# Optimization experiments

Hardware: AMD Instinct MI355X
Metric: run time of the kernel (lower is better)

## Reference

```python
import jax, jax.numpy as jnp
import numpy as np

L, H, D, M = 2, 8, 64, 64   # layers, heads, query dim, value dim
DM = H * M                  # d_model = 512
FF = 1024                   # feed-forward dim
B, S, F_IN = 8, 4096, 586   # batch, seq_len, input feature dim
EPS_ATTN = 1e-6             # fast_transformers LinearAttention eps
EPS_LN = 1e-5               # torch LayerNorm default eps


def setup_inputs() -> dict:
    key = jax.random.key(0)
    ks = jax.random.split(key, 16)
    p = lambda k, shape: jax.random.normal(k, shape, jnp.float32) * 0.02
    return {
        "embeddings": jax.random.normal(ks[0], (B, S, F_IN), jnp.float32),
        "W0": p(ks[1], (F_IN, DM)), "b0": jnp.zeros((DM,), jnp.float32),
        "Wq": p(ks[2], (L, DM, DM)), "bq": jnp.zeros((L, DM), jnp.float32),
        "Wk": p(ks[3], (L, DM, DM)), "bk": jnp.zeros((L, DM), jnp.float32),
        "Wv": p(ks[4], (L, DM, DM)), "bv": jnp.zeros((L, DM), jnp.float32),
        "Wo": p(ks[5], (L, DM, DM)), "bo": jnp.zeros((L, DM), jnp.float32),
        "ln1_s": jnp.ones((L, DM), jnp.float32), "ln1_b": jnp.zeros((L, DM), jnp.float32),
        "W1": p(ks[6], (L, DM, FF)), "b1": jnp.zeros((L, FF), jnp.float32),
        "W2": p(ks[7], (L, FF, DM)), "b2": jnp.zeros((L, DM), jnp.float32),
        "ln2_s": jnp.ones((L, DM), jnp.float32), "ln2_b": jnp.zeros((L, DM), jnp.float32),
        "lnf_s": jnp.ones((DM,), jnp.float32), "lnf_b": jnp.zeros((DM,), jnp.float32),
        "Wout": p(ks[8], (DM, 1)), "bout": jnp.zeros((1,), jnp.float32),
    }


def _ln(x, s, b):
    mu = x.mean(-1, keepdims=True)
    var = ((x - mu) ** 2).mean(-1, keepdims=True)
    return (x - mu) * jax.lax.rsqrt(var + EPS_LN) * s + b


def _feat(x):
    # elu feature map of fast_transformers linear attention
    return jax.nn.elu(x) + 1.0


def reference(embeddings, W0, b0, Wq, bq, Wk, bk, Wv, bv, Wo, bo,
              ln1_s, ln1_b, W1, b1, W2, b2, ln2_s, ln2_b,
              lnf_s, lnf_b, Wout, bout):
    x = embeddings @ W0 + b0                       # [B,S,DM]
    Bn, Sn = x.shape[0], x.shape[1]
    for l in range(L):
        q = _feat((x @ Wq[l] + bq[l]).reshape(Bn, Sn, H, D))
        k = _feat((x @ Wk[l] + bk[l]).reshape(Bn, Sn, H, D))
        v = (x @ Wv[l] + bv[l]).reshape(Bn, Sn, H, M)
        # non-causal linear attention: O(S) in sequence length
        kv = jnp.einsum("bshd,bshm->bhdm", k, v)                    # [B,H,D,M]
        z = 1.0 / (jnp.einsum("blhd,bhd->blh", q, k.sum(1)) + EPS_ATTN)
        a = jnp.einsum("blhd,bhdm,blh->blhm", q, kv, z).reshape(Bn, Sn, DM)
        x = x + a @ Wo[l] + bo[l]                  # residual (dropout=0 eval)
        x = _ln(x, ln1_s[l], ln1_b[l])
        y = jax.nn.relu(x @ W1[l] + b1[l]) @ W2[l] + b2[l]
        x = _ln(x + y, ln2_s[l], ln2_b[l])
    x = _ln(x, lnf_s, lnf_b)                        # final encoder LayerNorm
    return (x @ Wout + bout)[..., 0]                # squeeze -> [B,S]
```

## Files before the change

### kernel.cpp

```cpp
#include <hip/hip_runtime.h>
#include <hip/hip_bf16.h>
#include <math.h>

typedef unsigned short u16;
typedef short s16x8 __attribute__((ext_vector_type(8)));
typedef float f32x4 __attribute__((ext_vector_type(4)));

#define BS_   32768
#define SEQ_  4096
#define DM_   512
#define FF_   1024
#define FIN_  586
#define FINP_ 640
#define PADE  264

__device__ __forceinline__ u16 f2b(float f) {
    __hip_bfloat16 h = __float2bfloat16(f);
    return *reinterpret_cast<u16*>(&h);
}
__device__ __forceinline__ float b2f(u16 h) {
    union { unsigned u; float f; } a; a.u = ((unsigned)h) << 16;
    return a.f;
}

typedef __attribute__((address_space(1))) const unsigned gu32;
typedef __attribute__((address_space(3))) unsigned lu32;
__device__ __forceinline__ void glds16(const void* g, void* l) {
    __builtin_amdgcn_global_load_lds((gu32*)g, (lu32*)l, 16, 0, 0);
}

__device__ __forceinline__ void tr_tile(const float* __restrict__ W, u16* __restrict__ Wt,
                                        int K, int N, int Kpad, int tidx, int ktiles,
                                        float (*t)[33]) {
    int kb = (tidx % ktiles) << 5, nb = (tidx / ktiles) << 5;
    int tx = threadIdx.x, ty = threadIdx.y;
#pragma unroll
    for (int j = 0; j < 32; j += 8) {
        int k = kb + ty + j;
        t[ty + j][tx] = (k < K) ? W[(size_t)k * N + nb + tx] : 0.f;
    }
    __syncthreads();
#pragma unroll
    for (int j = 0; j < 32; j += 8) {
        Wt[(size_t)(nb + ty + j) * Kpad + kb + tx] = f2b(t[tx][ty + j]);
    }
}

__global__ void k_tr_all(const float* __restrict__ W0, const float* __restrict__ Wq,
                         const float* __restrict__ Wk, const float* __restrict__ Wv,
                         const float* __restrict__ Wo, const float* __restrict__ W1,
                         const float* __restrict__ W2,
                         u16* __restrict__ W0t, u16* __restrict__ Wqkv,
                         u16* __restrict__ Wot, u16* __restrict__ W1t,
                         u16* __restrict__ W2t) {
    __shared__ float t[32][33];
    int b = blockIdx.x;
    if (b < 320) { tr_tile(W0, W0t, FIN_, DM_, FINP_, b, 20, t); return; }
    b -= 320;
    int l = b >> 11;
    int r = b & 2047;
    if (r < 768) {
        int sel = r >> 8, ti = r & 255;
        const float* src = sel == 0 ? Wq : (sel == 1 ? Wk : Wv);
        tr_tile(src + (size_t)l * 262144, Wqkv + (size_t)l * 786432 + (size_t)sel * 262144,
                512, 512, 512, ti, 16, t);
    } else if (r < 1024) {
        tr_tile(Wo + (size_t)l * 262144, Wot + (size_t)l * 262144, 512, 512, 512, r - 768, 16, t);
    } else if (r < 1536) {
        tr_tile(W1 + (size_t)l * 524288, W1t + (size_t)l * 524288, 512, 1024, 512, r - 1024, 16, t);
    } else {
        tr_tile(W2 + (size_t)l * 524288, W2t + (size_t)l * 524288, 1024, 512, 1024, r - 1536, 32, t);
    }
}

__global__ __launch_bounds__(256)
void k_emb(const float* __restrict__ E, u16* __restrict__ Ep) {
    const int total8 = BS_ * (FINP_ / 8);
    for (int i = blockIdx.x * 256 + threadIdx.x; i < total8; i += gridDim.x * 256) {
        int rr = i / (FINP_ / 8), c = (i % (FINP_ / 8)) * 8;
        const float* rp = E + (size_t)rr * FIN_ + c;
        s16x8 o;
#pragma unroll
        for (int e = 0; e < 8; ++e) {
            float v = (c + e < FIN_) ? rp[e] : 0.f;
            o[e] = (short)f2b(v);
        }
        *(s16x8*)(Ep + (size_t)rr * FINP_ + c) = o;
    }
}

template<int EPI>
__global__ __launch_bounds__(512, 2)
void k_gemm(const u16* __restrict__ A, const u16* __restrict__ Bt,
            const float* __restrict__ bias0, const float* __restrict__ bias1,
            const float* __restrict__ bias2,
            const u16* __restrict__ resid,
            u16* __restrict__ out0, u16* __restrict__ out1, u16* __restrict__ out2,
            int M, int N, int K, int NT) {
    __shared__ __align__(16) u16 smem[65536];

    const int nwg = gridDim.x;
    const int cpx = nwg >> 3;
    const int wg = (blockIdx.x & 7) * cpx + (blockIdx.x >> 3);
    const int mt = wg / NT, ntl = wg - mt * NT;
    const int m0 = mt << 8, n0 = ntl << 8;
    const int tid = threadIdx.x;
    const int wid = tid >> 6, l = tid & 63;
    const int wr = wid >> 2, wc = wid & 3;
    const int lr = l & 15, lg = l >> 4;

    const int srow = tid >> 3;
    const int gchunk = (((tid & 7) ^ (srow & 7)) & 7) << 3;
    const u16* Abase = A + (size_t)(m0 + srow) * K + gchunk;
    const u16* Bbase = Bt + (size_t)(n0 + srow) * K + gchunk;

    auto stageA = [&](int d, int tt) {
        u16* dst = smem + d * 16384 + tid * 8;
        const u16* src = Abase + (size_t)tt * 64;
#pragma unroll
        for (int hg = 0; hg < 4; ++hg)
            glds16(src + (size_t)(hg * 64) * K, dst + hg * 4096);
    };
    auto stageB = [&](int d, int tt) {
        u16* dst = smem + 32768 + d * 16384 + tid * 8;
        const u16* src = Bbase + (size_t)tt * 64;
#pragma unroll
        for (int hg = 0; hg < 4; ++hg)
            glds16(src + (size_t)(hg * 64) * K, dst + hg * 4096);
    };

    const int aswz0 = ((0 + lg) ^ (lr & 7)) << 3;
    const int aswz1 = ((4 + lg) ^ (lr & 7)) << 3;

    f32x4 acc[8][4] = {};
    const int ntile = K >> 6;

    stageA(0, 0);
    stageB(0, 0);
    __syncthreads();

    s16x8 bf0[4], bf1[4];
    for (int t = 0; t < ntile; ++t) {
        const int d = t & 1, nd = d ^ 1;
        const int abase = d * 16384 + wr * 8192;
        const int bbase = 32768 + d * 16384 + (wc >> 1) * 8192 + ((wc & 1) * 64 + lr) * 64;
#pragma unroll
        for (int q = 0; q < 4; ++q) {
            const int r0 = (2 * q) * 16 + lr;
            const int r1 = (2 * q + 1) * 16 + lr;
            s16x8 a00 = *(const s16x8*)(smem + abase + r0 * 64 + aswz0);
            s16x8 a01 = *(const s16x8*)(smem + abase + r0 * 64 + aswz1);
            s16x8 a10 = *(const s16x8*)(smem + abase + r1 * 64 + aswz0);
            s16x8 a11 = *(const s16x8*)(smem + abase + r1 * 64 + aswz1);
            if (q == 0) {
#pragma unroll
                for (int fc = 0; fc < 4; ++fc) {
                    bf0[fc] = *(const s16x8*)(smem + bbase + fc * 1024 + aswz0);
                    bf1[fc] = *(const s16x8*)(smem + bbase + fc * 1024 + aswz1);
                }
                if (t + 1 < ntile) stageA(nd, t + 1);
            } else if (q == 1) {
                if (t + 1 < ntile) stageB(nd, t + 1);
            }
            __builtin_amdgcn_s_setprio(1);
#pragma unroll
            for (int fc = 0; fc < 4; ++fc) {
                acc[2 * q][fc]     = __builtin_amdgcn_mfma_f32_16x16x32_bf16(a00, bf0[fc], acc[2 * q][fc], 0, 0, 0);
                acc[2 * q][fc]     = __builtin_amdgcn_mfma_f32_16x16x32_bf16(a01, bf1[fc], acc[2 * q][fc], 0, 0, 0);
                acc[2 * q + 1][fc] = __builtin_amdgcn_mfma_f32_16x16x32_bf16(a10, bf0[fc], acc[2 * q + 1][fc], 0, 0, 0);
                acc[2 * q + 1][fc] = __builtin_amdgcn_mfma_f32_16x16x32_bf16(a11, bf1[fc], acc[2 * q + 1][fc], 0, 0, 0);
            }
            __builtin_amdgcn_s_setprio(0);
            if (q < 3) __builtin_amdgcn_s_barrier();
            else __syncthreads();
        }
    }

    const int seg = (EPI == 1) ? (n0 >> 9) : 0;
    const float* bias = (EPI == 1) ? (seg == 0 ? bias0 : (seg == 1 ? bias1 : bias2)) : bias0;
    u16* dst = (EPI == 1) ? (seg == 0 ? out0 : (seg == 1 ? out1 : out2)) : out0;
    const int ldo = (EPI == 1) ? 512 : N;
    const int ncol0 = (EPI == 1) ? (n0 & 511) : n0;

#pragma unroll
    for (int pass = 0; pass < 2; ++pass) {
        if (wr == pass) {
#pragma unroll
            for (int fc = 0; fc < 4; ++fc) {
                const int col = wc * 64 + fc * 16 + lr;
                const float bv = bias[ncol0 + col];
#pragma unroll
                for (int fr = 0; fr < 8; ++fr)
#pragma unroll
                    for (int r = 0; r < 4; ++r) {
                        const int row = fr * 16 + (lg << 2) + r;
                        smem[row * PADE + col] = f2b(acc[fr][fc][r] + bv);
                    }
            }
        }
        __syncthreads();
        const int rbase = m0 + (pass << 7);
#pragma unroll
        for (int it = 0; it < 8; ++it) {
            const int idx = it * 512 + tid;
            const int row = idx >> 5;
            const int c8 = (idx & 31) << 3;
            s16x8 v8 = *(const s16x8*)(smem + row * PADE + c8);
            size_t gaddr = (size_t)(rbase + row) * ldo + ncol0 + c8;
            s16x8 o = v8;
            if constexpr (EPI == 1) {
                if (seg < 2) {
#pragma unroll
                    for (int e = 0; e < 8; ++e) {
                        float v = b2f((u16)v8[e]);
                        v = (v > 0.f) ? v + 1.f : __expf(v);
                        o[e] = (short)f2b(v);
                    }
                }
            } else if constexpr (EPI == 2) {
                s16x8 rv = *(const s16x8*)(resid + gaddr);
#pragma unroll
                for (int e = 0; e < 8; ++e)
                    o[e] = (short)f2b(b2f((u16)v8[e]) + b2f((u16)rv[e]));
            } else if constexpr (EPI == 3) {
#pragma unroll
                for (int e = 0; e < 8; ++e)
                    o[e] = (short)f2b(fmaxf(b2f((u16)v8[e]), 0.f));
            }
            *(s16x8*)(dst + gaddr) = o;
        }
        __syncthreads();
    }
}

__global__ __launch_bounds__(256)
void k_kv(const u16* __restrict__ kb_, const u16* __restrict__ vb_,
          float* __restrict__ kvp, float* __restrict__ ksump) {
    __shared__ float sk[64 * 68], sv[64 * 68];
    int bh = blockIdx.x, b = bh >> 3, h = bh & 7;
    int ch = blockIdx.y;
    int tid = threadIdx.x;
    int d0 = (tid & 15) << 2, m0 = (tid >> 4) << 2;
    float acc[4][4] = {};
    float ks[4] = {0.f, 0.f, 0.f, 0.f};
    size_t gbase = ((size_t)b * SEQ_ + (size_t)ch * 1024) * DM_ + h * 64;

    for (int st = 0; st < 1024; st += 64) {
#pragma unroll
        for (int i = 0; i < 2; ++i) {
            int li = tid + (i << 8);
            int r = li >> 3, c8 = (li & 7) << 3;
            s16x8 kv_ = *(const s16x8*)(kb_ + gbase + (size_t)(st + r) * DM_ + c8);
            s16x8 vv_ = *(const s16x8*)(vb_ + gbase + (size_t)(st + r) * DM_ + c8);
#pragma unroll
            for (int e = 0; e < 8; ++e) {
                sk[r * 68 + c8 + e] = b2f((u16)kv_[e]);
                sv[r * 68 + c8 + e] = b2f((u16)vv_[e]);
            }
        }
        __syncthreads();
        for (int s = 0; s < 64; ++s) {
            f32x4 kd = *(const f32x4*)(sk + s * 68 + d0);
            f32x4 vm = *(const f32x4*)(sv + s * 68 + m0);
#pragma unroll
            for (int i = 0; i < 4; ++i)
#pragma unroll
                for (int j = 0; j < 4; ++j) acc[i][j] += kd[i] * vm[j];
            if ((tid >> 4) == 0) { ks[0] += kd[0]; ks[1] += kd[1]; ks[2] += kd[2]; ks[3] += kd[3]; }
        }
        __syncthreads();
    }
    float* kvo = kvp + ((size_t)ch * 64 + bh) * 4096;
#pragma unroll
    for (int i = 0; i < 4; ++i)
#pragma unroll
        for (int j = 0; j < 4; ++j) kvo[(d0 + i) * 64 + m0 + j] = acc[i][j];
    if ((tid >> 4) == 0) {
        float* kso = ksump + ((size_t)ch * 64 + bh) * 64;
#pragma unroll
        for (int e = 0; e < 4; ++e) kso[d0 + e] = ks[e];
    }
}

__global__ __launch_bounds__(256)
void k_attn(const u16* __restrict__ qb_, const float* __restrict__ kvp,
            const float* __restrict__ ksump, u16* __restrict__ ab_) {
    __shared__ float skv[64 * 64];
    __shared__ float sq[64 * 65];
    __shared__ float sks[64];
    int tid = threadIdx.x;
    int bh = blockIdx.y, b = bh >> 3, h = bh & 7;
    int s0 = blockIdx.x << 6;

    for (int i = tid; i < 4096; i += 256) {
        float v = 0.f;
#pragma unroll
        for (int c = 0; c < 4; ++c) v += kvp[((size_t)c * 64 + bh) * 4096 + i];
        skv[i] = v;
    }
    if (tid < 64) {
        float v = 0.f;
#pragma unroll
        for (int c = 0; c < 4; ++c) v += ksump[((size_t)c * 64 + bh) * 64 + tid];
        sks[tid] = v;
    }
#pragma unroll
    for (int i = 0; i < 2; ++i) {
        int li = tid + (i << 8);
        int r = li >> 3, c8 = (li & 7) << 3;
        s16x8 v = *(const s16x8*)(qb_ + ((size_t)b * SEQ_ + s0 + r) * DM_ + h * 64 + c8);
#pragma unroll
        for (int e = 0; e < 8; ++e) sq[r * 65 + c8 + e] = b2f((u16)v[e]);
    }
    __syncthreads();

    int sl = tid >> 2, m0 = (tid & 3) << 4;
    float den = 0.f;
    for (int d = 0; d < 64; ++d) den += sq[sl * 65 + d] * sks[d];
    float z = 1.f / (den + 1e-6f);

    float acc[16] = {};
    for (int d = 0; d < 64; ++d) {
        float qv = sq[sl * 65 + d];
        const f32x4* kp = (const f32x4*)(skv + d * 64 + m0);
#pragma unroll
        for (int j4 = 0; j4 < 4; ++j4) {
            f32x4 kv4 = kp[j4];
#pragma unroll
            for (int e = 0; e < 4; ++e) acc[j4 * 4 + e] += qv * kv4[e];
        }
    }
    u16* op = ab_ + ((size_t)b * SEQ_ + s0 + sl) * DM_ + h * 64 + m0;
    s16x8 o0, o1;
#pragma unroll
    for (int e = 0; e < 8; ++e) o0[e] = (short)f2b(acc[e] * z);
#pragma unroll
    for (int e = 0; e < 8; ++e) o1[e] = (short)f2b(acc[8 + e] * z);
    *(s16x8*)op = o0;
    *(s16x8*)(op + 8) = o1;
}

__global__ __launch_bounds__(256)
void k_ln(const u16* __restrict__ in, const float* __restrict__ g,
          const float* __restrict__ be, u16* __restrict__ xb) {
    int row = blockIdx.x * 4 + (threadIdx.x >> 6);
    int l = threadIdx.x & 63;
    s16x8 raw = *(const s16x8*)(in + (size_t)row * DM_ + l * 8);
    float x[8];
#pragma unroll
    for (int e = 0; e < 8; ++e) x[e] = b2f((u16)raw[e]);
    float sum = 0.f;
#pragma unroll
    for (int e = 0; e < 8; ++e) sum += x[e];
#pragma unroll
    for (int off = 32; off > 0; off >>= 1) sum += __shfl_xor(sum, off);
    float mu = sum * (1.f / DM_);
    float sq = 0.f;
#pragma unroll
    for (int e = 0; e < 8; ++e) { float d = x[e] - mu; sq += d * d; }
#pragma unroll
    for (int off = 32; off > 0; off >>= 1) sq += __shfl_xor(sq, off);
    float rs = rsqrtf(sq * (1.f / DM_) + 1e-5f);
    int c = l * 8;
    const f32x4* gp = (const f32x4*)(g + c);
    const f32x4* bp = (const f32x4*)(be + c);
    f32x4 g0 = gp[0], g1 = gp[1], e0 = bp[0], e1 = bp[1];
    s16x8 pk;
#pragma unroll
    for (int e = 0; e < 4; ++e) pk[e] = (short)f2b((x[e] - mu) * rs * g0[e] + e0[e]);
#pragma unroll
    for (int e = 0; e < 4; ++e) pk[4 + e] = (short)f2b((x[4 + e] - mu) * rs * g1[e] + e1[e]);
    *(s16x8*)(xb + (size_t)row * DM_ + c) = pk;
}

__global__ __launch_bounds__(256)
void k_ln2f(const u16* __restrict__ in, const float* __restrict__ g2,
            const float* __restrict__ b2_, const float* __restrict__ gf,
            const float* __restrict__ bf_, const float* __restrict__ wout,
            const float* __restrict__ bout, float* __restrict__ out) {
    int row = blockIdx.x * 4 + (threadIdx.x >> 6);
    int l = threadIdx.x & 63;
    s16x8 raw = *(const s16x8*)(in + (size_t)row * DM_ + l * 8);
    float x[8];
#pragma unroll
    for (int e = 0; e < 8; ++e) x[e] = b2f((u16)raw[e]);
    float sum = 0.f;
#pragma unroll
    for (int e = 0; e < 8; ++e) sum += x[e];
#pragma unroll
    for (int off = 32; off > 0; off >>= 1) sum += __shfl_xor(sum, off);
    float mu = sum * (1.f / DM_);
    float sq = 0.f;
#pragma unroll
    for (int e = 0; e < 8; ++e) { float d = x[e] - mu; sq += d * d; }
#pragma unroll
    for (int off = 32; off > 0; off >>= 1) sq += __shfl_xor(sq, off);
    float rs = rsqrtf(sq * (1.f / DM_) + 1e-5f);
    int c = l * 8;
    float t[8];
#pragma unroll
    for (int e = 0; e < 8; ++e) t[e] = (x[e] - mu) * rs * g2[c + e] + b2_[c + e];
    float sum2 = 0.f;
#pragma unroll
    for (int e = 0; e < 8; ++e) sum2 += t[e];
#pragma unroll
    for (int off = 32; off > 0; off >>= 1) sum2 += __shfl_xor(sum2, off);
    float mu2 = sum2 * (1.f / DM_);
    float sq2 = 0.f;
#pragma unroll
    for (int e = 0; e < 8; ++e) { float d = t[e] - mu2; sq2 += d * d; }
#pragma unroll
    for (int off = 32; off > 0; off >>= 1) sq2 += __shfl_xor(sq2, off);
    float rs2 = rsqrtf(sq2 * (1.f / DM_) + 1e-5f);
    float p = 0.f;
#pragma unroll
    for (int e = 0; e < 8; ++e)
        p += ((t[e] - mu2) * rs2 * gf[c + e] + bf_[c + e]) * wout[c + e];
#pragma unroll
    for (int off = 32; off > 0; off >>= 1) p += __shfl_xor(p, off);
    if (l == 0) out[row] = p + bout[0];
}

extern "C" void kernel_launch(void* const* d_in, const int* in_sizes, int n_in,
                              void* d_out, int out_size, void* d_ws, size_t ws_size,
                              hipStream_t stream) {
    const float* emb   = (const float*)d_in[0];
    const float* W0    = (const float*)d_in[1];
    const float* b0    = (const float*)d_in[2];
    const float* Wq    = (const float*)d_in[3];
    const float* bq    = (const float*)d_in[4];
    const float* Wk    = (const float*)d_in[5];
    const float* bk    = (const float*)d_in[6];
    const float* Wv    = (const float*)d_in[7];
    const float* bv    = (const float*)d_in[8];
    const float* Wo    = (const float*)d_in[9];
    const float* bo    = (const float*)d_in[10];
    const float* ln1s  = (const float*)d_in[11];
    const float* ln1b  = (const float*)d_in[12];
    const float* W1    = (const float*)d_in[13];
    const float* b1    = (const float*)d_in[14];
    const float* W2    = (const float*)d_in[15];
    const float* b2    = (const float*)d_in[16];
    const float* ln2s  = (const float*)d_in[17];
    const float* ln2b  = (const float*)d_in[18];
    const float* lnfs  = (const float*)d_in[19];
    const float* lnfb  = (const float*)d_in[20];
    const float* Wout  = (const float*)d_in[21];
    const float* bout  = (const float*)d_in[22];
    float* out = (float*)d_out;

    char* ws = (char*)d_ws;
    size_t off = 0;
    auto alloc = [&](size_t bytes) -> void* {
        void* p = ws + off;
        off += (bytes + 255) & ~(size_t)255;
        return p;
    };
    u16* xb   = (u16*)alloc((size_t)BS_ * DM_ * 2);
    u16* qb   = (u16*)alloc((size_t)BS_ * DM_ * 2);
    u16* kb   = (u16*)alloc((size_t)BS_ * DM_ * 2);
    u16* vb   = (u16*)alloc((size_t)BS_ * DM_ * 2);
    float* kvp   = (float*)alloc((size_t)4 * 64 * 4096 * 4);
    float* ksump = (float*)alloc((size_t)4 * 64 * 64 * 4);
    u16* wp   = (u16*)alloc((size_t)4521984 * 2);

    u16* rb   = qb;
    u16* ab   = vb;
    u16* h1b  = kb;
    u16* embp = kb;

    u16* W0t  = wp;
    u16* Wqkv = wp + 327680;
    u16* Wot  = Wqkv + 2 * 786432;
    u16* W1t  = Wot + 2 * 262144;
    u16* W2t  = W1t + 2 * 524288;

    k_tr_all<<<4416, dim3(32, 8), 0, stream>>>(W0, Wq, Wk, Wv, Wo, W1, W2,
                                               W0t, Wqkv, Wot, W1t, W2t);
    k_emb<<<2560, 256, 0, stream>>>(emb, embp);

    k_gemm<0><<<256, 512, 0, stream>>>(embp, W0t, b0, nullptr, nullptr,
                                       nullptr, xb, nullptr, nullptr, BS_, DM_, FINP_, 2);

    for (int l = 0; l < 2; ++l) {
        k_gemm<1><<<768, 512, 0, stream>>>(xb, Wqkv + (size_t)l * 786432,
                                           bq + l * 512, bk + l * 512, bv + l * 512,
                                           nullptr, qb, kb, vb, BS_, 1536, 512, 6);
        k_kv<<<dim3(64, 4), 256, 0, stream>>>(kb, vb, kvp, ksump);
        k_attn<<<dim3(64, 64), 256, 0, stream>>>(qb, kvp, ksump, ab);
        k_gemm<2><<<256, 512, 0, stream>>>(ab, Wot + (size_t)l * 262144,
                                           bo + l * 512, nullptr, nullptr,
                                           xb, rb, nullptr, nullptr, BS_, 512, 512, 2);
        k_ln<<<8192, 256, 0, stream>>>(rb, ln1s + l * 512, ln1b + l * 512, xb);
        k_gemm<3><<<512, 512, 0, stream>>>(xb, W1t + (size_t)l * 524288,
                                           b1 + l * 1024, nullptr, nullptr,
                                           nullptr, h1b, nullptr, nullptr, BS_, 1024, 512, 4);
        k_gemm<2><<<256, 512, 0, stream>>>(h1b, W2t + (size_t)l * 524288,
                                           b2 + l * 512, nullptr, nullptr,
                                           xb, rb, nullptr, nullptr, BS_, 512, 1024, 2);
        if (l == 0)
            k_ln<<<8192, 256, 0, stream>>>(rb, ln2s, ln2b, xb);
        else
            k_ln2f<<<8192, 256, 0, stream>>>(rb, ln2s + 512, ln2b + 512,
                                             lnfs, lnfb, Wout, bout, out);
    }
}
```

Before: 709.9 us.

## Split GEMM tile staging into waves with fine-grained vmcnt waits

Reorders the global-to-LDS staging of the next K tile into two groups (A rows 0/2 plus all of B, then A rows 1/3). Per-quarter barriers and the end-of-tile __syncthreads are replaced by explicit s_waitcnt vmcnt waits plus barriers at the start of the tile and before the q=2 quarter. The first half of the tile can therefore start computing before the second A half has landed. MFMA issue order is also interleaved so consecutive instructions target different accumulators, which reduces dependency stalls. The risk is that the hand-counted vmcnt values and barrier placement must exactly match the outstanding loads, or LDS could be read before it is written or overwritten while still in use.

```diff
diff --git a/kernel.cpp b/kernel.cpp
--- a/kernel.cpp
+++ b/kernel.cpp
@@ -114,19 +114,20 @@
     const u16* Abase = A + (size_t)(m0 + srow) * K + gchunk;
     const u16* Bbase = Bt + (size_t)(n0 + srow) * K + gchunk;
 
-    auto stageA = [&](int d, int tt) {
-        u16* dst = smem + d * 16384 + tid * 8;
-        const u16* src = Abase + (size_t)tt * 64;
-#pragma unroll
-        for (int hg = 0; hg < 4; ++hg)
-            glds16(src + (size_t)(hg * 64) * K, dst + hg * 4096);
+    auto stA = [&](int d, int tt, int h) {
+        glds16(Abase + (size_t)tt * 64 + (size_t)(h * 64) * K,
+               smem + d * 16384 + h * 4096 + tid * 8);
     };
-    auto stageB = [&](int d, int tt) {
-        u16* dst = smem + 32768 + d * 16384 + tid * 8;
-        const u16* src = Bbase + (size_t)tt * 64;
-#pragma unroll
-        for (int hg = 0; hg < 4; ++hg)
-            glds16(src + (size_t)(hg * 64) * K, dst + hg * 4096);
+    auto stB = [&](int d, int tt, int h) {
+        glds16(Bbase + (size_t)tt * 64 + (size_t)(h * 64) * K,
+               smem + 32768 + d * 16384 + h * 4096 + tid * 8);
+    };
+    auto stage6 = [&](int d, int tt) {
+        stA(d, tt, 0); stA(d, tt, 2);
+        stB(d, tt, 0); stB(d, tt, 1); stB(d, tt, 2); stB(d, tt, 3);
+    };
+    auto stage2 = [&](int d, int tt) {
+        stA(d, tt, 1); stA(d, tt, 3);
     };
 
     const int aswz0 = ((0 + lg) ^ (lr & 7)) << 3;
@@ -135,17 +136,27 @@
     f32x4 acc[8][4] = {};
     const int ntile = K >> 6;
 
-    stageA(0, 0);
-    stageB(0, 0);
-    __syncthreads();
+    stage6(0, 0);
+    stage2(0, 0);
 
     s16x8 bf0[4], bf1[4];
     for (int t = 0; t < ntile; ++t) {
         const int d = t & 1, nd = d ^ 1;
         const int abase = d * 16384 + wr * 8192;
         const int bbase = 32768 + d * 16384 + (wc >> 1) * 8192 + ((wc & 1) * 64 + lr) * 64;
+
+        asm volatile("s_waitcnt vmcnt(2)" ::: "memory");
+        __builtin_amdgcn_s_barrier();
+        __builtin_amdgcn_sched_barrier(0);
+
 #pragma unroll
         for (int q = 0; q < 4; ++q) {
+            if (q == 2) {
+                if (t + 1 < ntile) asm volatile("s_waitcnt vmcnt(8)" ::: "memory");
+                else               asm volatile("s_waitcnt vmcnt(0)" ::: "memory");
+                __builtin_amdgcn_s_barrier();
+                __builtin_amdgcn_sched_barrier(0);
+            }
             const int r0 = (2 * q) * 16 + lr;
             const int r1 = (2 * q + 1) * 16 + lr;
             s16x8 a00 = *(const s16x8*)(smem + abase + r0 * 64 + aswz0);
@@ -158,23 +169,25 @@
                     bf0[fc] = *(const s16x8*)(smem + bbase + fc * 1024 + aswz0);
                     bf1[fc] = *(const s16x8*)(smem + bbase + fc * 1024 + aswz1);
                 }
-                if (t + 1 < ntile) stageA(nd, t + 1);
+                if (t + 1 < ntile) stage6(nd, t + 1);
             } else if (q == 1) {
-                if (t + 1 < ntile) stageB(nd, t + 1);
+                if (t + 1 < ntile) stage2(nd, t + 1);
             }
             __builtin_amdgcn_s_setprio(1);
 #pragma unroll
             for (int fc = 0; fc < 4; ++fc) {
                 acc[2 * q][fc]     = __builtin_amdgcn_mfma_f32_16x16x32_bf16(a00, bf0[fc], acc[2 * q][fc], 0, 0, 0);
+                acc[2 * q + 1][fc] = __builtin_amdgcn_mfma_f32_16x16x32_bf16(a10, bf0[fc], acc[2 * q + 1][fc], 0, 0, 0);
+            }
+#pragma unroll
+            for (int fc = 0; fc < 4; ++fc) {
                 acc[2 * q][fc]     = __builtin_amdgcn_mfma_f32_16x16x32_bf16(a01, bf1[fc], acc[2 * q][fc], 0, 0, 0);
-                acc[2 * q + 1][fc] = __builtin_amdgcn_mfma_f32_16x16x32_bf16(a10, bf0[fc], acc[2 * q + 1][fc], 0, 0, 0);
                 acc[2 * q + 1][fc] = __builtin_amdgcn_mfma_f32_16x16x32_bf16(a11, bf1[fc], acc[2 * q + 1][fc], 0, 0, 0);
             }
             __builtin_amdgcn_s_setprio(0);
-            if (q < 3) __builtin_amdgcn_s_barrier();
-            else __syncthreads();
-        }
-    }
+        }
+    }
+    __syncthreads();
 
     const int seg = (EPI == 1) ? (n0 >> 9) : 0;
     const float* bias = (EPI == 1) ? (seg == 0 ? bias0 : (seg == 1 ? bias1 : bias2)) : bias0;
```

Result: no change. 714.1 us (+0.6%).
